# Kernel optimization log

Measured on AMD Instinct MI355X. Metric: run time of the kernel, lower is better.

The kernel has to match this reference:

```python
import jax, jax.numpy as jnp
import numpy as np

M = 4                 # margin order (init kwarg m=4)
LAMB = 1000.0         # it=0: max(lambda_min, lambda_max/(1+gamma*0)**power) = 1000
B, D, C = 512, 256, 100000


def setup_inputs() -> dict:
    key = jax.random.key(0)
    k1, k2, k3 = jax.random.split(key, 3)
    x = jax.random.normal(k1, (B, D), dtype=jnp.float32)
    # kaiming_uniform_(weight, a=1.0): bound = sqrt(6/((1+a^2)*fan_in)) = sqrt(3/D)
    bound = float(np.sqrt(3.0 / D))
    weight = jax.random.uniform(k2, (C, D), dtype=jnp.float32, minval=-bound, maxval=bound)
    y = jax.random.randint(k3, (B,), 0, C)
    return {"x": x, "weight": weight, "y": y}


def reference(x, weight, y):
    # weight row-normalization (normalize=True path, done in-place in torch)
    wl = jnp.sqrt(jnp.sum(weight * weight, axis=1, keepdims=True))
    w = weight / wl                                  # (C, D), unit rows -> wlen == 1
    xlen = jnp.sqrt(jnp.sum(x * x, axis=1, keepdims=True))   # (B, 1)
    cos = jnp.clip((x @ w.T) / xlen, -1.0, 1.0)      # (B, C) cos_theta
    # m=4 Chebyshev: cos(4t) = 8c^4 - 8c^2 + 1
    c2 = cos * cos
    cos_m = 8.0 * c2 * c2 - 8.0 * c2 + 1.0
    k = jnp.floor(M * jnp.arccos(cos) / jnp.pi)      # (B, C)
    sign = 1.0 - 2.0 * (k % 2.0)                     # (-1)**k
    phi = sign * cos_m - 2.0 * k
    feat = cos * xlen
    onehot = jax.nn.one_hot(y, w.shape[0], dtype=feat.dtype)  # (B, C)
    # at label positions: feat <- (lamb*feat + phi*xlen) / (1+lamb)
    feat = feat + onehot * ((phi * xlen - feat) / (1.0 + LAMB))
    return feat
```

## Files before the change

### kernel.cpp

```cpp
#include <hip/hip_runtime.h>
#include <hip/hip_bf16.h>

#define B_DIM 512
#define D_DIM 256
#define C_DIM 100000
#define LAMB 1000.0f

using bf16x8 = __attribute__((ext_vector_type(8))) short;
using f32x4  = __attribute__((ext_vector_type(4))) float;

__device__ __forceinline__ short f2bf(float f) {
  unsigned u = __builtin_bit_cast(unsigned, f);
  u += 0x7FFFu + ((u >> 16) & 1u);
  return (short)(u >> 16);
}

__device__ __forceinline__ void gload_lds16(const void* g, void* l) {
  __builtin_amdgcn_global_load_lds(
      (__attribute__((address_space(1))) void*)g,
      (__attribute__((address_space(3))) void*)l, 16, 0, 0);
}

__global__ __launch_bounds__(256) void prep_x(const float* __restrict__ x,
                                              unsigned short* __restrict__ x_swz,
                                              float* __restrict__ xlen) {
  int wv = threadIdx.x >> 6, lane = threadIdx.x & 63;
  int row = blockIdx.x * 4 + wv;
  float4 v = *(const float4*)(x + row * D_DIM + lane * 4);
  float ss = v.x * v.x + v.y * v.y + v.z * v.z + v.w * v.w;
#pragma unroll
  for (int m = 1; m < 64; m <<= 1) ss += __shfl_xor(ss, m);
  if (lane == 0) xlen[row] = sqrtf(ss);
  ushort4 u;
  u.x = (unsigned short)f2bf(v.x);
  u.y = (unsigned short)f2bf(v.y);
  u.z = (unsigned short)f2bf(v.z);
  u.w = (unsigned short)f2bf(v.w);
  int byteoff = row * 512 + ((lane * 8) ^ ((row & 7) << 4));
  *(ushort4*)((char*)x_swz + byteoff) = u;
}

__global__ __launch_bounds__(256) void gemm_bf16(
    const float* __restrict__ W, const unsigned short* __restrict__ xb,
    const float* __restrict__ xlen, float* __restrict__ out) {
  __shared__ unsigned short xs[2][32 * 256];
  __shared__ float xlen_s[B_DIM];

  const int tid = threadIdx.x;
  const int lane = tid & 63, wv = tid >> 6;
  const int l15 = lane & 15, g = lane >> 4;
  const int bn0 = blockIdx.x * 128 + wv * 32;

  for (int i = tid; i < B_DIM; i += 256) xlen_s[i] = xlen[i];

#pragma unroll
  for (int i = 0; i < 4; ++i)
    gload_lds16((const char*)xb + i * 4096 + tid * 16,
                (char*)xs[0] + i * 4096 + wv * 1024);

  bf16x8 fw[2][8];
  float invw4[2][4];
#pragma unroll
  for (int it = 0; it < 2; ++it) {
    int col = bn0 + it * 16 + l15;
    if (col >= C_DIM) col = C_DIM - 1;
    const float* wr = W + (size_t)col * D_DIM + g * 8;
    float ss = 0.f;
#pragma unroll
    for (int kg = 0; kg < 8; ++kg) {
      float4 a = *(const float4*)(wr + kg * 32);
      float4 b = *(const float4*)(wr + kg * 32 + 4);
      ss += a.x * a.x + a.y * a.y + a.z * a.z + a.w * a.w
          + b.x * b.x + b.y * b.y + b.z * b.z + b.w * b.w;
      bf16x8 f;
      f[0] = f2bf(a.x); f[1] = f2bf(a.y); f[2] = f2bf(a.z); f[3] = f2bf(a.w);
      f[4] = f2bf(b.x); f[5] = f2bf(b.y); f[6] = f2bf(b.z); f[7] = f2bf(b.w);
      fw[it][kg] = f;
    }
    ss += __shfl_xor(ss, 16);
    ss += __shfl_xor(ss, 32);
    float iw = 1.0f / sqrtf(ss);
#pragma unroll
    for (int r = 0; r < 4; ++r) invw4[it][r] = __shfl(iw, g * 4 + r);
  }

  __syncthreads();

  int buf = 0;
  for (int chunk = 0; chunk < 16; ++chunk) {
    if (chunk < 15) {
#pragma unroll
      for (int i = 0; i < 4; ++i)
        gload_lds16((const char*)xb + (chunk + 1) * 16384 + i * 4096 + tid * 16,
                    (char*)xs[buf ^ 1] + i * 4096 + wv * 1024);
    }
    __builtin_amdgcn_sched_barrier(0);

#pragma unroll
    for (int jtl = 0; jtl < 2; ++jtl) {
      const int xrow = chunk * 32 + jtl * 16 + l15;
      const float xl = xlen_s[xrow];
      const char* xp = (const char*)xs[buf] + (jtl * 16 + l15) * 512;
      const int swz = (l15 & 7) << 4;
      bf16x8 fx[8];
#pragma unroll
      for (int kg = 0; kg < 8; ++kg)
        fx[kg] = *(const bf16x8*)(xp + ((kg * 64 + g * 16) ^ swz));

      f32x4 acc0 = {}, acc1 = {};
#pragma unroll
      for (int kg = 0; kg < 8; ++kg) {
        acc0 = __builtin_amdgcn_mfma_f32_16x16x32_bf16(fw[0][kg], fx[kg], acc0, 0, 0, 0);
        acc1 = __builtin_amdgcn_mfma_f32_16x16x32_bf16(fw[1][kg], fx[kg], acc1, 0, 0, 0);
      }

#pragma unroll
      for (int it = 0; it < 2; ++it) {
        const f32x4& a = it ? acc1 : acc0;
        int wc = bn0 + it * 16 + g * 4;
        if (wc < C_DIM) {
          float4 v;
          v.x = fminf(fmaxf(a[0] * invw4[it][0], -xl), xl);
          v.y = fminf(fmaxf(a[1] * invw4[it][1], -xl), xl);
          v.z = fminf(fmaxf(a[2] * invw4[it][2], -xl), xl);
          v.w = fminf(fmaxf(a[3] * invw4[it][3], -xl), xl);
          *(float4*)(out + (size_t)xrow * C_DIM + wc) = v;
        }
      }
    }

    __builtin_amdgcn_sched_barrier(0);
    asm volatile("s_waitcnt vmcnt(4)" ::: "memory");
    __builtin_amdgcn_s_barrier();
    __builtin_amdgcn_sched_barrier(0);
    buf ^= 1;
  }
}

__global__ __launch_bounds__(256) void fix_labels(const float* __restrict__ x,
                                                  const float* __restrict__ W,
                                                  const int* __restrict__ y,
                                                  float* __restrict__ out) {
  int wv = threadIdx.x >> 6, lane = threadIdx.x & 63;
  int b = blockIdx.x * 4 + wv;
  int c = y[b];
  float4 wvv = *(const float4*)(W + (size_t)c * D_DIM + lane * 4);
  float4 xv  = *(const float4*)(x + b * D_DIM + lane * 4);
  float dt = wvv.x * xv.x + wvv.y * xv.y + wvv.z * xv.z + wvv.w * xv.w;
  float sw = wvv.x * wvv.x + wvv.y * wvv.y + wvv.z * wvv.z + wvv.w * wvv.w;
  float sx = xv.x * xv.x + xv.y * xv.y + xv.z * xv.z + xv.w * xv.w;
#pragma unroll
  for (int m = 1; m < 64; m <<= 1) {
    dt += __shfl_xor(dt, m);
    sw += __shfl_xor(sw, m);
    sx += __shfl_xor(sx, m);
  }
  if (lane == 0) {
    float xl = sqrtf(sx), wl = sqrtf(sw);
    float cth = dt / (xl * wl);
    cth = fminf(fmaxf(cth, -1.f), 1.f);
    float c2 = cth * cth;
    float cm = 8.f * c2 * c2 - 8.f * c2 + 1.f;
    float k = floorf(4.0f * acosf(cth) / 3.14159265358979323846f);
    float sgn = (((int)k) & 1) ? -1.f : 1.f;
    float phi = sgn * cm - 2.f * k;
    float feat = cth * xl;
    out[(size_t)b * C_DIM + c] = feat + (phi * xl - feat) / (1.f + LAMB);
  }
}

extern "C" void kernel_launch(void* const* d_in, const int* in_sizes, int n_in,
                              void* d_out, int out_size, void* d_ws, size_t ws_size,
                              hipStream_t stream) {
  const float* x = (const float*)d_in[0];
  const float* W = (const float*)d_in[1];
  const int*   y = (const int*)d_in[2];
  float* out = (float*)d_out;

  unsigned short* xb = (unsigned short*)d_ws;
  float* xlen = (float*)((char*)d_ws + B_DIM * D_DIM * 2);

  prep_x<<<B_DIM / 4, 256, 0, stream>>>(x, xb, xlen);
  gemm_bf16<<<(C_DIM + 127) / 128, 256, 0, stream>>>(W, xb, xlen, out);
  fix_labels<<<B_DIM / 4, 256, 0, stream>>>(x, W, y, out);
}
```

Before: 96.54 us.

## Stage weight rows through LDS with coalesced loads and prenormalize before bf16

Weight rows are now fetched into LDS with global_load_lds, one row per 1KB contiguous transfer, instead of strided per-lane float4 loads. Each row is normalized in registers before conversion to bf16, which removes the per-output inverse-norm multiply in the epilogue. The chunk loop's explicit vmcnt wait plus raw barrier is replaced with __syncthreads, which waits for all outstanding loads and so may serialize the x prefetch with compute. The weight staging runs serially in four waits-for-zero steps, which adds latency to the prologue.

```diff
diff --git a/kernel.cpp b/kernel.cpp
--- a/kernel.cpp
+++ b/kernel.cpp
@@ -53,37 +53,55 @@
 
   for (int i = tid; i < B_DIM; i += 256) xlen_s[i] = xlen[i];
 
+  char* wsbase = (char*)xs + wv * 8192;
+  bf16x8 fw[2][8];
+#pragma unroll
+  for (int s = 0; s < 4; ++s) {
+    const int it = s >> 1, half = s & 1;
+    const int colbase = bn0 + it * 16 + half * 8;
+#pragma unroll
+    for (int i = 0; i < 8; ++i) {
+      int c = colbase + i; if (c > C_DIM - 1) c = C_DIM - 1;
+      gload_lds16((const char*)(W + (size_t)c * D_DIM) + lane * 16,
+                  wsbase + i * 1024);
+    }
+    asm volatile("s_waitcnt vmcnt(0)" ::: "memory");
+    __builtin_amdgcn_sched_barrier(0);
+    const int cl = l15 - half * 8;
+    const bool active = (cl >= 0) && (cl < 8);
+    const char* colp = wsbase + (active ? cl : 0) * 1024 + g * 32;
+    float ss = 0.f;
+#pragma unroll
+    for (int kg = 0; kg < 8; ++kg) {
+      float4 a = *(const float4*)(colp + kg * 128);
+      float4 b = *(const float4*)(colp + kg * 128 + 16);
+      ss += a.x * a.x + a.y * a.y + a.z * a.z + a.w * a.w
+          + b.x * b.x + b.y * b.y + b.z * b.z + b.w * b.w;
+    }
+    ss += __shfl_xor(ss, 16);
+    ss += __shfl_xor(ss, 32);
+    const float iw = 1.0f / sqrtf(ss);
+#pragma unroll
+    for (int kg = 0; kg < 8; ++kg) {
+      float4 a = *(const float4*)(colp + kg * 128);
+      float4 b = *(const float4*)(colp + kg * 128 + 16);
+      bf16x8 f;
+      f[0] = f2bf(a.x * iw); f[1] = f2bf(a.y * iw);
+      f[2] = f2bf(a.z * iw); f[3] = f2bf(a.w * iw);
+      f[4] = f2bf(b.x * iw); f[5] = f2bf(b.y * iw);
+      f[6] = f2bf(b.z * iw); f[7] = f2bf(b.w * iw);
+      if (active) fw[it][kg] = f;
+    }
+    asm volatile("s_waitcnt lgkmcnt(0)" ::: "memory");
+    __builtin_amdgcn_sched_barrier(0);
+  }
+
+  __syncthreads();
+
 #pragma unroll
   for (int i = 0; i < 4; ++i)
     gload_lds16((const char*)xb + i * 4096 + tid * 16,
                 (char*)xs[0] + i * 4096 + wv * 1024);
-
-  bf16x8 fw[2][8];
-  float invw4[2][4];
-#pragma unroll
-  for (int it = 0; it < 2; ++it) {
-    int col = bn0 + it * 16 + l15;
-    if (col >= C_DIM) col = C_DIM - 1;
-    const float* wr = W + (size_t)col * D_DIM + g * 8;
-    float ss = 0.f;
-#pragma unroll
-    for (int kg = 0; kg < 8; ++kg) {
-      float4 a = *(const float4*)(wr + kg * 32);
-      float4 b = *(const float4*)(wr + kg * 32 + 4);
-      ss += a.x * a.x + a.y * a.y + a.z * a.z + a.w * a.w
-          + b.x * b.x + b.y * b.y + b.z * b.z + b.w * b.w;
-      bf16x8 f;
-      f[0] = f2bf(a.x); f[1] = f2bf(a.y); f[2] = f2bf(a.z); f[3] = f2bf(a.w);
-      f[4] = f2bf(b.x); f[5] = f2bf(b.y); f[6] = f2bf(b.z); f[7] = f2bf(b.w);
-      fw[it][kg] = f;
-    }
-    ss += __shfl_xor(ss, 16);
-    ss += __shfl_xor(ss, 32);
-    float iw = 1.0f / sqrtf(ss);
-#pragma unroll
-    for (int r = 0; r < 4; ++r) invw4[it][r] = __shfl(iw, g * 4 + r);
-  }
-
   __syncthreads();
 
   int buf = 0;
@@ -120,19 +138,16 @@
         int wc = bn0 + it * 16 + g * 4;
         if (wc < C_DIM) {
           float4 v;
-          v.x = fminf(fmaxf(a[0] * invw4[it][0], -xl), xl);
-          v.y = fminf(fmaxf(a[1] * invw4[it][1], -xl), xl);
-          v.z = fminf(fmaxf(a[2] * invw4[it][2], -xl), xl);
-          v.w = fminf(fmaxf(a[3] * invw4[it][3], -xl), xl);
+          v.x = fminf(fmaxf(a[0], -xl), xl);
+          v.y = fminf(fmaxf(a[1], -xl), xl);
+          v.z = fminf(fmaxf(a[2], -xl), xl);
+          v.w = fminf(fmaxf(a[3], -xl), xl);
           *(float4*)(out + (size_t)xrow * C_DIM + wc) = v;
         }
       }
     }
 
-    __builtin_amdgcn_sched_barrier(0);
-    asm volatile("s_waitcnt vmcnt(4)" ::: "memory");
-    __builtin_amdgcn_s_barrier();
-    __builtin_amdgcn_sched_barrier(0);
+    __syncthreads();
     buf ^= 1;
   }
 }
```

Result: slower. 105.6 us (+9.4%).

## Use 4-stage 16-row LDS ring with prefetch distance two for x tiles

Applied to the files above, without the earlier changes.

Replaces the double-buffered 32-row x chunks with a four-slot ring of 16-row chunks, prefetching two chunks ahead. Each iteration waits on a partial vmcnt and a barrier before consuming its slot, so more global-to-LDS loads stay in flight while MFMAs and output stores proceed. The vmcnt accounting is hand-tuned and depends on how many loads and stores are outstanding; it also adds one barrier per 16 rows instead of per 32 rows.

```diff
diff --git a/kernel.cpp b/kernel.cpp
--- a/kernel.cpp
+++ b/kernel.cpp
@@ -43,7 +43,7 @@
 __global__ __launch_bounds__(256) void gemm_bf16(
     const float* __restrict__ W, const unsigned short* __restrict__ xb,
     const float* __restrict__ xlen, float* __restrict__ out) {
-  __shared__ unsigned short xs[2][32 * 256];
+  __shared__ unsigned short xs[4][16 * 256];
   __shared__ float xlen_s[B_DIM];
 
   const int tid = threadIdx.x;
@@ -54,9 +54,11 @@
   for (int i = tid; i < B_DIM; i += 256) xlen_s[i] = xlen[i];
 
 #pragma unroll
-  for (int i = 0; i < 4; ++i)
-    gload_lds16((const char*)xb + i * 4096 + tid * 16,
-                (char*)xs[0] + i * 4096 + wv * 1024);
+  for (int c = 0; c < 2; ++c)
+#pragma unroll
+    for (int i = 0; i < 2; ++i)
+      gload_lds16((const char*)xb + c * 8192 + wv * 2048 + i * 1024 + lane * 16,
+                  (char*)xs[c] + wv * 2048 + i * 1024 + lane * 16);
 
   bf16x8 fw[2][8];
   float invw4[2][4];
@@ -84,56 +86,54 @@
     for (int r = 0; r < 4; ++r) invw4[it][r] = __shfl(iw, g * 4 + r);
   }
 
-  __syncthreads();
-
-  int buf = 0;
-  for (int chunk = 0; chunk < 16; ++chunk) {
-    if (chunk < 15) {
+  for (int k = 0; k < 32; ++k) {
+    if (k < 30) {
 #pragma unroll
-      for (int i = 0; i < 4; ++i)
-        gload_lds16((const char*)xb + (chunk + 1) * 16384 + i * 4096 + tid * 16,
-                    (char*)xs[buf ^ 1] + i * 4096 + wv * 1024);
+      for (int i = 0; i < 2; ++i)
+        gload_lds16((const char*)xb + (k + 2) * 8192 + wv * 2048 + i * 1024 + lane * 16,
+                    (char*)xs[(k + 2) & 3] + wv * 2048 + i * 1024 + lane * 16);
     }
     __builtin_amdgcn_sched_barrier(0);
 
+    if (k == 0 || k == 31)
+      asm volatile("s_waitcnt vmcnt(4)" ::: "memory");
+    else if (k == 1 || k == 30)
+      asm volatile("s_waitcnt vmcnt(6)" ::: "memory");
+    else
+      asm volatile("s_waitcnt vmcnt(8)" ::: "memory");
+    __builtin_amdgcn_s_barrier();
+    __builtin_amdgcn_sched_barrier(0);
+
+    const int row = k * 16 + l15;
+    const float xl = xlen_s[row];
+    const char* xp = (const char*)xs[k & 3] + l15 * 512;
+    const int swz = (l15 & 7) << 4;
+    bf16x8 fx[8];
 #pragma unroll
-    for (int jtl = 0; jtl < 2; ++jtl) {
-      const int xrow = chunk * 32 + jtl * 16 + l15;
-      const float xl = xlen_s[xrow];
-      const char* xp = (const char*)xs[buf] + (jtl * 16 + l15) * 512;
-      const int swz = (l15 & 7) << 4;
-      bf16x8 fx[8];
+    for (int kg = 0; kg < 8; ++kg)
+      fx[kg] = *(const bf16x8*)(xp + ((kg * 64 + g * 16) ^ swz));
+
+    f32x4 acc0 = {}, acc1 = {};
 #pragma unroll
-      for (int kg = 0; kg < 8; ++kg)
-        fx[kg] = *(const bf16x8*)(xp + ((kg * 64 + g * 16) ^ swz));
+    for (int kg = 0; kg < 8; ++kg) {
+      acc0 = __builtin_amdgcn_mfma_f32_16x16x32_bf16(fw[0][kg], fx[kg], acc0, 0, 0, 0);
+      acc1 = __builtin_amdgcn_mfma_f32_16x16x32_bf16(fw[1][kg], fx[kg], acc1, 0, 0, 0);
+    }
 
-      f32x4 acc0 = {}, acc1 = {};
+    const size_t orow = (size_t)row * C_DIM;
 #pragma unroll
-      for (int kg = 0; kg < 8; ++kg) {
-        acc0 = __builtin_amdgcn_mfma_f32_16x16x32_bf16(fw[0][kg], fx[kg], acc0, 0, 0, 0);
-        acc1 = __builtin_amdgcn_mfma_f32_16x16x32_bf16(fw[1][kg], fx[kg], acc1, 0, 0, 0);
-      }
-
-#pragma unroll
-      for (int it = 0; it < 2; ++it) {
-        const f32x4& a = it ? acc1 : acc0;
-        int wc = bn0 + it * 16 + g * 4;
-        if (wc < C_DIM) {
-          float4 v;
-          v.x = fminf(fmaxf(a[0] * invw4[it][0], -xl), xl);
-          v.y = fminf(fmaxf(a[1] * invw4[it][1], -xl), xl);
-          v.z = fminf(fmaxf(a[2] * invw4[it][2], -xl), xl);
-          v.w = fminf(fmaxf(a[3] * invw4[it][3], -xl), xl);
-          *(float4*)(out + (size_t)xrow * C_DIM + wc) = v;
-        }
+    for (int it = 0; it < 2; ++it) {
+      const f32x4& a = it ? acc1 : acc0;
+      int wc = bn0 + it * 16 + g * 4;
+      if (wc < C_DIM) {
+        float4 v;
+        v.x = fminf(fmaxf(a[0] * invw4[it][0], -xl), xl);
+        v.y = fminf(fmaxf(a[1] * invw4[it][1], -xl), xl);
+        v.z = fminf(fmaxf(a[2] * invw4[it][2], -xl), xl);
+        v.w = fminf(fmaxf(a[3] * invw4[it][3], -xl), xl);
+        *(float4*)(out + orow + wc) = v;
       }
     }
-
-    __builtin_amdgcn_sched_barrier(0);
-    asm volatile("s_waitcnt vmcnt(4)" ::: "memory");
-    __builtin_amdgcn_s_barrier();
-    __builtin_amdgcn_sched_barrier(0);
-    buf ^= 1;
   }
 }
 
```

Result: faster. 93.75 us (-2.9%).
